# Performance work log

Hardware: AMD Instinct MI355X
Metric: run time of the kernel (lower is better)

The kernel has to match this reference:

```python
import jax, jax.numpy as jnp
import numpy as np

TOPK = 100  # hardcoded in Block: kNNAttention(..., topk=100)
EPS = 1e-5  # torch LayerNorm default


def layer_norm(x, w, b):
    m = jnp.mean(x, axis=-1, keepdims=True)
    v = jnp.mean(jnp.square(x - m), axis=-1, keepdims=True)
    return (x - m) * jax.lax.rsqrt(v + EPS) * w + b


def setup_inputs() -> dict:
    key = jax.random.key(0)
    ks = jax.random.split(key, 8)
    B, N, C, H = 32, 512, 768, 12
    hid = 4 * C
    s_in = 1.0 / np.sqrt(C)
    s_hid = 1.0 / np.sqrt(hid)
    return {
        "x": jax.random.normal(ks[0], (B, N, C), jnp.float32),
        "islast": 0,
        "ln1_w": jnp.ones((C,), jnp.float32),
        "ln1_b": jnp.zeros((C,), jnp.float32),
        "qkv_w": jax.random.normal(ks[1], (3 * C, C), jnp.float32) * s_in,  # qkv_bias=False
        "proj_w": jax.random.normal(ks[2], (C, C), jnp.float32) * s_in,
        "proj_b": jnp.zeros((C,), jnp.float32),
        "ln2_w": jnp.ones((C,), jnp.float32),
        "ln2_b": jnp.zeros((C,), jnp.float32),
        "fc1_w": jax.random.normal(ks[3], (hid, C), jnp.float32) * s_in,
        "fc1_b": jnp.zeros((hid,), jnp.float32),
        "fc2_w": jax.random.normal(ks[4], (C, hid), jnp.float32) * s_hid,
        "fc2_b": jnp.zeros((C,), jnp.float32),
    }


def reference(x, islast, ln1_w, ln1_b, qkv_w, proj_w, proj_b, ln2_w, ln2_b, fc1_w, fc1_b, fc2_w, fc2_b):
    B, N, C = x.shape
    H = 12
    D = C // H
    scale = D ** -0.5

    # --- kNN attention on norm1(x) ---
    xn = layer_norm(x, ln1_w, ln1_b)
    qkv = (xn @ qkv_w.T).reshape(B, N, 3, H, D)
    q, k, v = (qkv[:, :, 0].transpose(0, 2, 1, 3),
               qkv[:, :, 1].transpose(0, 2, 1, 3),
               qkv[:, :, 2].transpose(0, 2, 1, 3))  # [B,H,N,D]
    attn = jnp.einsum("bhnd,bhmd->bhnm", q, k) * scale  # [B,H,N,N]
    if not bool(islast):
        # top-k mask per query row (equivalent to topk + scatter mask; ties measure-zero for floats)
        kth = jax.lax.top_k(attn, TOPK)[0][..., -1:]
        attn = jnp.where(attn >= kth, attn, -jnp.inf)
    attn = jax.nn.softmax(attn, axis=-1)
    out = jnp.einsum("bhnm,bhmd->bhnd", attn, v).transpose(0, 2, 1, 3).reshape(B, N, C)
    out = out @ proj_w.T + proj_b
    x = x + out  # residual (drop_path/dropout = 0, eval)

    # --- MLP on norm2(x) ---
    xn2 = layer_norm(x, ln2_w, ln2_b)
    h = jax.nn.gelu(xn2 @ fc1_w.T + fc1_b, approximate=False)
    x = x + (h @ fc2_w.T + fc2_b)
    return x, attn
```

## Files before the change

kernel.cpp:

```cpp
#include <hip/hip_runtime.h>
#include <hip/hip_bf16.h>
#include <math.h>

using bf16 = __hip_bfloat16;
typedef __attribute__((ext_vector_type(8))) short bh8;
typedef __attribute__((ext_vector_type(4))) float f4;

static const long long X_ELEMS = 12582912LL;

enum { EPI_F32 = 0, EPI_BIAS_RES = 2, EPI_BIAS_GELU = 3, EPI_QKV = 4, EPI_PV = 5 };

__device__ __forceinline__ float fin(float v) {
  return (fabsf(v) < 1e30f) ? v : 0.f;
}
__device__ __forceinline__ unsigned short f2bf(float f) {
  bf16 h = __float2bfloat16(f);
  return *reinterpret_cast<unsigned short*>(&h);
}
__device__ __forceinline__ uint4 pack8(float4 a, float4 b) {
  union { uint4 u; unsigned short h[8]; } r;
  r.h[0] = f2bf(a.x); r.h[1] = f2bf(a.y); r.h[2] = f2bf(a.z); r.h[3] = f2bf(a.w);
  r.h[4] = f2bf(b.x); r.h[5] = f2bf(b.y); r.h[6] = f2bf(b.z); r.h[7] = f2bf(b.w);
  return r.u;
}
__device__ __forceinline__ void gl_lds16(const bf16* g, unsigned short* l) {
  __builtin_amdgcn_global_load_lds((const __attribute__((address_space(1))) void*)g,
                                   (__attribute__((address_space(3))) void*)l, 16, 0, 0);
}

__global__ __launch_bounds__(256) void cast_all(const float* __restrict__ qkv_w,
    const float* __restrict__ proj_w, const float* __restrict__ fc1_w,
    const float* __restrict__ fc2_w, bf16* __restrict__ dst) {
  int i = blockIdx.x * 256 + threadIdx.x;
  const float* s; int base;
  if (i < 442368)       { s = qkv_w;  base = 0; }
  else if (i < 589824)  { s = proj_w; base = 442368; }
  else if (i < 1179648) { s = fc1_w;  base = 589824; }
  else                  { s = fc2_w;  base = 1179648; }
  float4 f = ((const float4*)s)[i - base];
  union { uint2 u; unsigned short h[4]; } r;
  r.h[0] = f2bf(f.x); r.h[1] = f2bf(f.y); r.h[2] = f2bf(f.z); r.h[3] = f2bf(f.w);
  ((uint2*)dst)[i] = r.u;
}

__global__ __launch_bounds__(256) void ln_kernel(const float* __restrict__ x,
    const float* __restrict__ w, const float* __restrict__ bi, bf16* __restrict__ out) {
  int row = blockIdx.x; int t = threadIdx.x;
  const float* xr = x + (size_t)row * 768;
  float v0 = xr[t], v1 = xr[t + 256], v2 = xr[t + 512];
  float s = v0 + v1 + v2;
  float s2 = v0 * v0 + v1 * v1 + v2 * v2;
  for (int off = 32; off; off >>= 1) { s += __shfl_down(s, off); s2 += __shfl_down(s2, off); }
  __shared__ float ls[4], ls2[4];
  int wid = t >> 6, lane = t & 63;
  if (lane == 0) { ls[wid] = s; ls2[wid] = s2; }
  __syncthreads();
  float S = ls[0] + ls[1] + ls[2] + ls[3];
  float S2 = ls2[0] + ls2[1] + ls2[2] + ls2[3];
  float mean = S * (1.0f / 768.0f);
  float var = S2 * (1.0f / 768.0f) - mean * mean;
  float rstd = rsqrtf(fmaxf(var, 0.f) + 1e-5f);
  bf16* orow = out + (size_t)row * 768;
  orow[t]       = __float2bfloat16((v0 - mean) * rstd * w[t]       + bi[t]);
  orow[t + 256] = __float2bfloat16((v1 - mean) * rstd * w[t + 256] + bi[t + 256]);
  orow[t + 512] = __float2bfloat16((v2 - mean) * rstd * w[t + 512] + bi[t + 512]);
}

template<int BN, int EPI, bool AF32>
__global__ __launch_bounds__(256)
void gemm_bt(const void* __restrict__ A, const bf16* __restrict__ B, void* __restrict__ Cout,
             int M, int N, int K,
             long long sA, long long sB, long long sC,
             const float* __restrict__ bias, const float* __restrict__ resid, float alpha,
             bf16* __restrict__ qo, bf16* __restrict__ ko, bf16* __restrict__ vo) {
  const int BM = 128, BK = 32;
  const int WN = BN / 2;
  const int NB = WN / 16;
  __shared__ unsigned short As[BM * BK];
  __shared__ unsigned short Bs[BN * BK];
  int t = threadIdx.x;
  int wid = t >> 6, lane = t & 63;
  int wm = wid >> 1, wn = wid & 1;
  int m0 = blockIdx.y * BM;
  int n0 = blockIdx.x * BN;
  int z = blockIdx.z;

  f4 acc[4][NB];
#pragma unroll
  for (int i = 0; i < 4; i++)
#pragma unroll
    for (int j = 0; j < NB; j++) acc[i][j] = f4{0.f, 0.f, 0.f, 0.f};

  int rowT = t >> 2;
  int colT = (t & 3) * 8;
  int q16 = lane >> 4;
  int r16 = lane & 15;

  unsigned short* lA = As + (size_t)wid * 512;
  unsigned short* lB = Bs + (size_t)wid * 512;

  for (int k0 = 0; k0 < K; k0 += BK) {
    uint4 a0, a1;
    if (AF32) {
      const float* aP = (const float*)A + (long long)z * sA + (long long)(m0 + rowT) * K + (k0 + colT);
      float4 f0 = *(const float4*)aP, f1 = *(const float4*)(aP + 4);
      a0 = pack8(f0, f1);
      const float* aQ = aP + (long long)64 * K;
      f0 = *(const float4*)aQ; f1 = *(const float4*)(aQ + 4);
      a1 = pack8(f0, f1);
    }
    __syncthreads();
    if (AF32) {
      *(uint4*)&As[rowT * BK + colT] = a0;
      *(uint4*)&As[(rowT + 64) * BK + colT] = a1;
    } else {
      const bf16* aP = (const bf16*)A + (long long)z * sA + (long long)(m0 + rowT) * K + (k0 + colT);
      gl_lds16(aP, lA);
      gl_lds16(aP + (long long)64 * K, lA + 2048);
    }
    {
      const bf16* bP = B + (long long)z * sB + (long long)(n0 + rowT) * K + (k0 + colT);
      gl_lds16(bP, lB);
      if (BN == 128) gl_lds16(bP + (long long)64 * K, lB + 2048);
    }
    asm volatile("s_waitcnt vmcnt(0)" ::: "memory");
    __syncthreads();

    bh8 af[4], bfr[NB];
#pragma unroll
    for (int i = 0; i < 4; i++) {
      int r = wm * 64 + i * 16 + r16;
      af[i] = *(const bh8*)&As[r * BK + q16 * 8];
    }
#pragma unroll
    for (int j = 0; j < NB; j++) {
      int r = wn * WN + j * 16 + r16;
      bfr[j] = *(const bh8*)&Bs[r * BK + q16 * 8];
    }
#pragma unroll
    for (int i = 0; i < 4; i++)
#pragma unroll
      for (int j = 0; j < NB; j++)
        acc[i][j] = __builtin_amdgcn_mfma_f32_16x16x32_bf16(af[i], bfr[j], acc[i][j], 0, 0, 0);
  }

  long long cbase = (long long)z * sC;
#pragma unroll
  for (int i = 0; i < 4; i++) {
#pragma unroll
    for (int j = 0; j < NB; j++) {
#pragma unroll
      for (int r = 0; r < 4; r++) {
        int mg = m0 + wm * 64 + i * 16 + q16 * 4 + r;
        int ng = n0 + wn * WN + j * 16 + r16;
        float v = acc[i][j][r] * alpha;
        if (EPI == EPI_F32) {
          ((float*)Cout)[cbase + (long long)mg * N + ng] = fin(v);
        } else if (EPI == EPI_BIAS_RES) {
          long long idx = cbase + (long long)mg * N + ng;
          v += bias[ng] + resid[idx];
          ((float*)Cout)[idx] = fin(v);
        } else if (EPI == EPI_BIAS_GELU) {
          v = fin(v + bias[ng]);
          float g = 0.5f * v * (1.0f + erff(v * 0.70710678118654752f));
          ((bf16*)Cout)[cbase + (long long)mg * N + ng] = __float2bfloat16(g);
        } else if (EPI == EPI_QKV) {
          int b = mg >> 9, n = mg & 511;
          int which = ng / 768;
          int c = ng - which * 768;
          int h = c >> 6, d = c & 63;
          size_t zz = (size_t)(b * 12 + h);
          bf16 val = __float2bfloat16(fin(v));
          if (which == 0)      qo[zz * 32768 + n * 64 + d] = val;
          else if (which == 1) ko[zz * 32768 + n * 64 + d] = val;
          else                 vo[(zz * 64 + d) * 512 + n] = val;
        } else {
          int b = z / 12, h = z - b * 12;
          ((bf16*)Cout)[((size_t)(b * 512 + mg)) * 768 + h * 64 + ng] = __float2bfloat16(fin(v));
        }
      }
    }
  }
}

__global__ __launch_bounds__(256) void topk_softmax(float* __restrict__ S,
                                                    const int* __restrict__ islast) {
  int wid = threadIdx.x >> 6, lane = threadIdx.x & 63;
  long long row = (long long)blockIdx.x * 4 + wid;
  float* sr = S + row * 512;
  float4 va = ((const float4*)sr)[lane];
  float4 vb = ((const float4*)sr)[lane + 64];
  float v[8] = {va.x, va.y, va.z, va.w, vb.x, vb.y, vb.z, vb.w};
  unsigned key[8];
  float m = -1e30f;
#pragma unroll
  for (int e = 0; e < 8; e++) {
    if (!(v[e] >= -1e38f)) v[e] = -1e38f;
    unsigned u = __float_as_uint(v[e]);
    key[e] = (u & 0x80000000u) ? ~u : (u | 0x80000000u);
    m = fmaxf(m, v[e]);
  }
  for (int off = 32; off; off >>= 1) m = fmaxf(m, __shfl_xor(m, off));

  unsigned T = 0;
  if (*islast == 0) {
    for (int bit = 31; bit >= 0; --bit) {
      unsigned Tc = T | (1u << bit);
      int cnt = 0;
#pragma unroll
      for (int e = 0; e < 8; e++) cnt += __popcll(__ballot(key[e] >= Tc));
      if (cnt >= 100) T = Tc;
      if (cnt == 100) break;
    }
  }
  float p[8]; float Z = 0.f;
#pragma unroll
  for (int e = 0; e < 8; e++) { p[e] = (key[e] >= T) ? __expf(v[e] - m) : 0.f; Z += p[e]; }
  for (int off = 32; off; off >>= 1) Z += __shfl_xor(Z, off);
  float rz = (Z > 0.f) ? (1.0f / Z) : 0.f;
  ((float4*)sr)[lane]      = float4{p[0] * rz, p[1] * rz, p[2] * rz, p[3] * rz};
  ((float4*)sr)[lane + 64] = float4{p[4] * rz, p[5] * rz, p[6] * rz, p[7] * rz};
}

extern "C" void kernel_launch(void* const* d_in, const int* in_sizes, int n_in,
                              void* d_out, int out_size, void* d_ws, size_t ws_size,
                              hipStream_t stream) {
  const float* x      = (const float*)d_in[0];
  const int*   islast = (const int*)d_in[1];
  const float* ln1_w  = (const float*)d_in[2];
  const float* ln1_b  = (const float*)d_in[3];
  const float* qkv_w  = (const float*)d_in[4];
  const float* proj_w = (const float*)d_in[5];
  const float* proj_b = (const float*)d_in[6];
  const float* ln2_w  = (const float*)d_in[7];
  const float* ln2_b  = (const float*)d_in[8];
  const float* fc1_w  = (const float*)d_in[9];
  const float* fc1_b  = (const float*)d_in[10];
  const float* fc2_w  = (const float*)d_in[11];
  const float* fc2_b  = (const float*)d_in[12];

  char* ws = (char*)d_ws;
  bf16*  wqkv = (bf16*)(ws + 0LL);
  bf16*  wproj= (bf16*)(ws + 3538944LL);
  bf16*  wfc1 = (bf16*)(ws + 4718592LL);
  bf16*  wfc2 = (bf16*)(ws + 9437184LL);
  bf16*  q    = (bf16*)(ws + 14155776LL);
  bf16*  kk   = (bf16*)(ws + 39321600LL);
  bf16*  vT   = (bf16*)(ws + 64487424LL);
  bf16*  AO   = q;
  bf16*  Hbuf = q;
  float* X1   = (float*)(ws + 39321600LL);

  float* outX    = (float*)d_out;
  float* outAttn = outX + X_ELEMS;
  bf16*  XN  = (bf16*)outX;
  bf16*  XN2 = (bf16*)((char*)d_out + 25165824LL);

  cast_all<<<6912, 256, 0, stream>>>(qkv_w, proj_w, fc1_w, fc2_w, wqkv);
  ln_kernel<<<16384, 256, 0, stream>>>(x, ln1_w, ln1_b, XN);
  gemm_bt<128, EPI_QKV, false><<<dim3(18, 128, 1), 256, 0, stream>>>(
      XN, wqkv, nullptr, 16384, 2304, 768, 0, 0, 0, nullptr, nullptr, 1.0f, q, kk, vT);
  gemm_bt<128, EPI_F32, false><<<dim3(4, 4, 384), 256, 0, stream>>>(
      q, kk, outAttn, 512, 512, 64, 32768, 32768, 262144, nullptr, nullptr, 0.125f,
      nullptr, nullptr, nullptr);
  topk_softmax<<<49152, 256, 0, stream>>>(outAttn, islast);
  gemm_bt<64, EPI_PV, true><<<dim3(1, 4, 384), 256, 0, stream>>>(
      outAttn, vT, AO, 512, 64, 512, 262144, 32768, 0, nullptr, nullptr, 1.0f,
      nullptr, nullptr, nullptr);
  gemm_bt<128, EPI_BIAS_RES, false><<<dim3(6, 128, 1), 256, 0, stream>>>(
      AO, wproj, X1, 16384, 768, 768, 0, 0, 0, proj_b, x, 1.0f, nullptr, nullptr, nullptr);
  ln_kernel<<<16384, 256, 0, stream>>>(X1, ln2_w, ln2_b, XN2);
  for (int i = 0; i < 4; ++i) {
    const bf16* xn2c = XN2 + (long long)i * 4096 * 768;
    gemm_bt<128, EPI_BIAS_GELU, false><<<dim3(24, 32, 1), 256, 0, stream>>>(
        xn2c, wfc1, Hbuf, 4096, 3072, 768, 0, 0, 0, fc1_b, nullptr, 1.0f,
        nullptr, nullptr, nullptr);
    gemm_bt<128, EPI_BIAS_RES, false><<<dim3(6, 32, 1), 256, 0, stream>>>(
        Hbuf, wfc2, outX + (long long)i * 4096 * 768, 4096, 768, 3072, 0, 0, 0,
        fc2_b, X1 + (long long)i * 4096 * 768, 1.0f, nullptr, nullptr, nullptr);
  }
  (void)in_sizes; (void)n_in; (void)out_size; (void)ws_size;
}
```

Before: 1.451 ms.

## Fuse QK^T score computation with top-k softmax in LDS

Measured after the change: 1.522 ms. 4.9% more time.

```diff
diff --git a/kernel.cpp b/kernel.cpp
--- a/kernel.cpp
+++ b/kernel.cpp
@@ -183,43 +183,82 @@
   }
 }
 
-__global__ __launch_bounds__(256) void topk_softmax(float* __restrict__ S,
-                                                    const int* __restrict__ islast) {
-  int wid = threadIdx.x >> 6, lane = threadIdx.x & 63;
-  long long row = (long long)blockIdx.x * 4 + wid;
-  float* sr = S + row * 512;
-  float4 va = ((const float4*)sr)[lane];
-  float4 vb = ((const float4*)sr)[lane + 64];
-  float v[8] = {va.x, va.y, va.z, va.w, vb.x, vb.y, vb.z, vb.w};
-  unsigned key[8];
-  float m = -1e30f;
-#pragma unroll
-  for (int e = 0; e < 8; e++) {
-    if (!(v[e] >= -1e38f)) v[e] = -1e38f;
-    unsigned u = __float_as_uint(v[e]);
-    key[e] = (u & 0x80000000u) ? ~u : (u | 0x80000000u);
-    m = fmaxf(m, v[e]);
-  }
-  for (int off = 32; off; off >>= 1) m = fmaxf(m, __shfl_xor(m, off));
-
-  unsigned T = 0;
-  if (*islast == 0) {
-    for (int bit = 31; bit >= 0; --bit) {
-      unsigned Tc = T | (1u << bit);
-      int cnt = 0;
-#pragma unroll
-      for (int e = 0; e < 8; e++) cnt += __popcll(__ballot(key[e] >= Tc));
-      if (cnt >= 100) T = Tc;
-      if (cnt == 100) break;
-    }
-  }
-  float p[8]; float Z = 0.f;
-#pragma unroll
-  for (int e = 0; e < 8; e++) { p[e] = (key[e] >= T) ? __expf(v[e] - m) : 0.f; Z += p[e]; }
-  for (int off = 32; off; off >>= 1) Z += __shfl_xor(Z, off);
-  float rz = (Z > 0.f) ? (1.0f / Z) : 0.f;
-  ((float4*)sr)[lane]      = float4{p[0] * rz, p[1] * rz, p[2] * rz, p[3] * rz};
-  ((float4*)sr)[lane + 64] = float4{p[4] * rz, p[5] * rz, p[6] * rz, p[7] * rz};
+__global__ __launch_bounds__(256)
+void attn_topk(const bf16* __restrict__ q, const bf16* __restrict__ kk,
+               float* __restrict__ probs, const int* __restrict__ islast) {
+  __shared__ float S[32 * 512];
+  int t = threadIdx.x;
+  int wid = t >> 6, lane = t & 63;
+  int q16 = lane >> 4, r16 = lane & 15;
+  int g = blockIdx.x;
+  int xcd = g & 7, idx = g >> 3;
+  int z = xcd * 48 + (idx >> 4);
+  int qb = idx & 15;
+  long long zoff = (long long)z * 32768;
+
+  int qrow0 = qb * 32 + (wid >> 1) * 16;
+  int col0 = (wid & 1) * 256;
+
+  const bf16* qp = q + zoff + (long long)(qrow0 + r16) * 64 + q16 * 8;
+  union { uint4 u; bh8 h; } uq0, uq1;
+  uq0.u = *(const uint4*)qp;
+  uq1.u = *(const uint4*)(qp + 32);
+
+  for (int nb = 0; nb < 16; ++nb) {
+    int r = col0 + nb * 16 + r16;
+    const bf16* kp = kk + zoff + (long long)r * 64 + q16 * 8;
+    union { uint4 u; bh8 h; } uk0, uk1;
+    uk0.u = *(const uint4*)kp;
+    uk1.u = *(const uint4*)(kp + 32);
+    f4 a = f4{0.f, 0.f, 0.f, 0.f};
+    a = __builtin_amdgcn_mfma_f32_16x16x32_bf16(uq0.h, uk0.h, a, 0, 0, 0);
+    a = __builtin_amdgcn_mfma_f32_16x16x32_bf16(uq1.h, uk1.h, a, 0, 0, 0);
+    int srow = (wid >> 1) * 16 + q16 * 4;
+    int scol = col0 + nb * 16 + r16;
+#pragma unroll
+    for (int rr = 0; rr < 4; ++rr)
+      S[(srow + rr) * 512 + scol] = fin(a[rr] * 0.125f);
+  }
+  __syncthreads();
+
+  int isl = *islast;
+  for (int rp = 0; rp < 8; ++rp) {
+    int lrow = wid * 8 + rp;
+    const float* sr = S + lrow * 512;
+    float4 va = ((const float4*)sr)[lane];
+    float4 vb = ((const float4*)sr)[lane + 64];
+    float v[8] = {va.x, va.y, va.z, va.w, vb.x, vb.y, vb.z, vb.w};
+    unsigned key[8];
+    float m = -1e30f;
+#pragma unroll
+    for (int e = 0; e < 8; e++) {
+      if (!(v[e] >= -1e38f)) v[e] = -1e38f;
+      unsigned u = __float_as_uint(v[e]);
+      key[e] = (u & 0x80000000u) ? ~u : (u | 0x80000000u);
+      m = fmaxf(m, v[e]);
+    }
+    for (int off = 32; off; off >>= 1) m = fmaxf(m, __shfl_xor(m, off));
+
+    unsigned T = 0;
+    if (isl == 0) {
+      for (int bit = 31; bit >= 0; --bit) {
+        unsigned Tc = T | (1u << bit);
+        int cnt = 0;
+#pragma unroll
+        for (int e = 0; e < 8; e++) cnt += __popcll(__ballot(key[e] >= Tc));
+        if (cnt >= 100) T = Tc;
+        if (cnt == 100) break;
+      }
+    }
+    float p[8]; float Z = 0.f;
+#pragma unroll
+    for (int e = 0; e < 8; e++) { p[e] = (key[e] >= T) ? __expf(v[e] - m) : 0.f; Z += p[e]; }
+    for (int off = 32; off; off >>= 1) Z += __shfl_xor(Z, off);
+    float rz = (Z > 0.f) ? (1.0f / Z) : 0.f;
+    float* og = probs + (long long)z * 262144 + (long long)(qb * 32 + lrow) * 512;
+    ((float4*)og)[lane]      = float4{p[0] * rz, p[1] * rz, p[2] * rz, p[3] * rz};
+    ((float4*)og)[lane + 64] = float4{p[4] * rz, p[5] * rz, p[6] * rz, p[7] * rz};
+  }
 }
 
 extern "C" void kernel_launch(void* const* d_in, const int* in_sizes, int n_in,
@@ -260,10 +299,7 @@
   ln_kernel<<<16384, 256, 0, stream>>>(x, ln1_w, ln1_b, XN);
   gemm_bt<128, EPI_QKV, false><<<dim3(18, 128, 1), 256, 0, stream>>>(
       XN, wqkv, nullptr, 16384, 2304, 768, 0, 0, 0, nullptr, nullptr, 1.0f, q, kk, vT);
-  gemm_bt<128, EPI_F32, false><<<dim3(4, 4, 384), 256, 0, stream>>>(
-      q, kk, outAttn, 512, 512, 64, 32768, 32768, 262144, nullptr, nullptr, 0.125f,
-      nullptr, nullptr, nullptr);
-  topk_softmax<<<49152, 256, 0, stream>>>(outAttn, islast);
+  attn_topk<<<6144, 256, 0, stream>>>(q, kk, outAttn, islast);
   gemm_bt<64, EPI_PV, true><<<dim3(1, 4, 384), 256, 0, stream>>>(
       outAttn, vT, AO, 512, 64, 512, 262144, 32768, 0, nullptr, nullptr, 1.0f,
       nullptr, nullptr, nullptr);
```
